# Kernel optimization log

Measured on AMD Instinct MI355X. Metric: run time of the kernel, lower is better.

The kernel has to match this reference:

```python
import jax, jax.numpy as jnp
import numpy as np
import math

T = 2048; HID = 2048; H = 16; KV = 8; G = H // KV; D = 128
GH = 128; BS = 64; NB = T // BS
EPS = 1e-6; RATIO = 0.2; SCALE = 1.0 / math.sqrt(D)


def _rope_tables(length, dim, theta=1000000.0):
    inv = 1.0 / (theta ** (np.arange(0, dim, 2, dtype=np.float32) / dim))
    f = np.outer(np.arange(length, dtype=np.float32), inv)
    emb = np.concatenate([f, f], axis=-1)
    return jnp.asarray(np.cos(emb)), jnp.asarray(np.sin(emb))


def _rot_half(x):
    d = x.shape[-1] // 2
    return jnp.concatenate([-x[..., d:], x[..., :d]], axis=-1)


def _apply_rope(x, cos, sin):
    # x: [T, nH, D], cos/sin: [T, D] broadcast over head dim
    return x * cos[:, None, :] + _rot_half(x) * sin[:, None, :]


def _rmsnorm(x, w, eps=EPS):
    xf = x.astype(jnp.float32)
    v = jnp.mean(xf * xf, axis=-1, keepdims=True)
    return (w * (xf * jax.lax.rsqrt(v + eps))).astype(x.dtype)


def setup_inputs() -> dict:
    key = jax.random.key(0)
    ks = jax.random.split(key, 8)
    s = 0.02
    hidden_states = jax.random.normal(ks[0], (T, HID), jnp.float32)
    Wq = jax.random.normal(ks[1], (HID, H * D), jnp.float32) * s
    Wk = jax.random.normal(ks[2], (HID, KV * D), jnp.float32) * s
    Wv = jax.random.normal(ks[3], (HID, KV * D), jnp.float32) * s
    Wo = jax.random.normal(ks[4], (H * D, HID), jnp.float32) * s
    q_norm_w = jnp.ones((D,), jnp.float32)
    k_norm_w = jnp.ones((D,), jnp.float32)
    gate_wq = jax.random.normal(ks[5], (D, GH), jnp.float32) * s
    gate_wk = jax.random.normal(ks[6], (D, GH), jnp.float32) * s
    cos, sin = _rope_tables(T, D)
    cos_gq, sin_gq = _rope_tables(T, GH)
    cos_blk, sin_blk = _rope_tables(NB, GH)
    # causal block mask: query t may attend to key block j iff j <= t // BS
    block_attention_mask = (jnp.arange(T)[:, None] // BS) >= jnp.arange(NB)[None, :]
    return dict(hidden_states=hidden_states, Wq=Wq, Wk=Wk, Wv=Wv, Wo=Wo,
                q_norm_w=q_norm_w, k_norm_w=k_norm_w, gate_wq=gate_wq, gate_wk=gate_wk,
                cos=cos, sin=sin, cos_gq=cos_gq, sin_gq=sin_gq,
                cos_blk=cos_blk, sin_blk=sin_blk,
                block_attention_mask=block_attention_mask)


def reference(hidden_states, Wq, Wk, Wv, Wo, q_norm_w, k_norm_w, gate_wq, gate_wk,
              cos, sin, cos_gq, sin_gq, cos_blk, sin_blk, block_attention_mask):
    q = (hidden_states @ Wq).reshape(T, H, D)
    k = (hidden_states @ Wk).reshape(T, KV, D)
    v = (hidden_states @ Wv).reshape(T, KV, D)
    q = _rmsnorm(q, q_norm_w)
    k = _rmsnorm(k, k_norm_w)

    # ---- gate network on un-roped q/k: q-head avg-pool to KV heads, k avg-pool per block ----
    q_pool = q.reshape(T, KV, G, D).mean(axis=2)            # [T, KV, D]
    gq = _apply_rope(q_pool @ gate_wq, cos_gq, sin_gq)      # [T, KV, GH]
    k_blk = k.reshape(NB, BS, KV, D).mean(axis=1)           # [NB, KV, D]
    gk = _apply_rope(k_blk @ gate_wk, cos_blk, sin_blk)     # [NB, KV, GH]
    gate_scores = jnp.einsum('tkg,nkg->ktn', gq, gk) / math.sqrt(GH)  # [KV, T, NB]
    predict_mask = jnp.where(block_attention_mask[None], gate_scores, -1e9)

    # ---- main attention (RoPE + GQA causal softmax attention) ----
    qr = _apply_rope(q, cos, sin)
    kr = _apply_rope(k, cos, sin)
    kr_rep = jnp.repeat(kr, G, axis=1)                      # [T, H, D]
    v_rep = jnp.repeat(v, G, axis=1)
    logits = jnp.einsum('thd,shd->hts', qr, kr_rep) * SCALE  # [H, T, T]
    causal = jnp.tril(jnp.ones((T, T), bool))
    logits = jnp.where(causal[None], logits, -jnp.inf)
    probs = jax.nn.softmax(logits, axis=-1)
    attn_output = jnp.einsum('hts,shd->thd', probs, v_rep).reshape(T, H * D) @ Wo

    # ---- pooled ground-truth block mask: attention mass per key block ----
    pooled = probs.reshape(H, T, NB, BS).sum(axis=-1)        # [H, T, NB]
    gt = pooled.reshape(KV, G, T, NB).max(axis=1)            # max_pool3d over head groups -> [KV,T,NB]
    gt = jnp.where(block_attention_mask[None], gt, 0.0)
    gt = gt / (gt.sum(axis=-1, keepdims=True) + 1e-9)

    # ---- KLDiv gate loss on the tail slice (bsz = 1) ----
    start = int(T * RATIO)
    tgt = gt[:, start:, :]                                   # [KV, L, NB]
    logp = jax.nn.log_softmax(predict_mask[:, start:, :], axis=-1)
    safe_t = jnp.where(tgt > 0, tgt, 1.0)
    kl = jnp.where(tgt > 0, tgt * (jnp.log(safe_t) - logp), 0.0)
    gate_loss = kl.reshape(KV, -1).mean(axis=-1).sum()       # KLDivLoss(reduction='mean') per kv head, summed, /bsz(=1)
    return attn_output, gate_loss
```

## Files before the change

### kernel.cpp

```cpp
#include <hip/hip_runtime.h>

#define T_ 2048
#define HID_ 2048
#define H_ 16
#define KV_ 8
#define G_ 2
#define D_ 128
#define GH_ 128
#define BS_ 64
#define NB_ 32
#define START_ 409
#define TG0_ 384
#define SCALE_ 0.08838834764831845f
#define MFIX_ 8.0f

typedef __attribute__((ext_vector_type(8))) short short8_t;
typedef __attribute__((ext_vector_type(4))) float float4_t;
typedef __attribute__((ext_vector_type(8))) unsigned short ushort8_t;
typedef __attribute__((ext_vector_type(4))) unsigned short ushort4_t;

__device__ __forceinline__ float wave_sum(float v) {
#pragma unroll
  for (int o = 32; o > 0; o >>= 1) v += __shfl_xor(v, o, 64);
  return v;
}
__device__ __forceinline__ unsigned short f2bf(float x) {
  unsigned int u = __float_as_uint(x);
  unsigned int r = (u + 0x7fffu + ((u >> 16) & 1u)) >> 16;
  return (unsigned short)r;
}

__device__ __forceinline__ void gload16(const void* g, void* l) {
  __builtin_amdgcn_global_load_lds((const __attribute__((address_space(1))) unsigned int*)g,
                                   (__attribute__((address_space(3))) unsigned int*)l, 16, 0, 0);
}

__device__ __forceinline__ void castT_dev(const float* __restrict__ in,
                                          unsigned short* __restrict__ out, int K, int N,
                                          int ldin, int bx, int by,
                                          unsigned short (*tile)[72], int tid) {
  int k0 = by * 64, n0 = bx * 64;
  int tx = tid & 63, ty4 = tid >> 6;
#pragma unroll
  for (int i = 0; i < 16; ++i) {
    int ky = ty4 * 16 + i;
    tile[tx][ky] = f2bf(in[(size_t)(k0 + ky) * ldin + n0 + tx]);
  }
  __syncthreads();
#pragma unroll
  for (int i = 0; i < 16; ++i) {
    int ny = ty4 * 16 + i;
    out[(size_t)(n0 + ny) * K + k0 + tx] = tile[ny][tx];
  }
}

__global__ __launch_bounds__(256) void castT(const float* __restrict__ in,
                                             unsigned short* __restrict__ out,
                                             int K, int N, int ldin) {
  __shared__ unsigned short tile[64][72];
  castT_dev(in, out, K, N, ldin, blockIdx.x, blockIdx.y, tile, threadIdx.x);
}

__global__ __launch_bounds__(256) void prep_cast(const float* __restrict__ hs,
                                                 const float* __restrict__ Wq,
                                                 const float* __restrict__ Wk,
                                                 const float* __restrict__ Wv,
                                                 const float* __restrict__ Wo,
                                                 const float* __restrict__ gwq,
                                                 const float* __restrict__ gwk,
                                                 unsigned short* __restrict__ hsb,
                                                 unsigned short* __restrict__ WqkvT,
                                                 unsigned short* __restrict__ WoT,
                                                 unsigned short* __restrict__ gwqT,
                                                 unsigned short* __restrict__ gwkT) {
  __shared__ unsigned short tile[64][72];
  int id = blockIdx.x, tid = threadIdx.x;
  if (id < 4096) {
    int i = id * 256 + tid;
    float4 v = ((const float4*)hs)[i];
    ushort4_t o = {f2bf(v.x), f2bf(v.y), f2bf(v.z), f2bf(v.w)};
    *(ushort4_t*)(hsb + (size_t)i * 4) = o;
  } else if (id < 5120) {
    int t = id - 4096;
    castT_dev(Wq, WqkvT, 2048, 2048, 2048, t & 31, t >> 5, tile, tid);
  } else if (id < 5632) {
    int t = id - 5120;
    castT_dev(Wk, WqkvT + (size_t)2048 * 2048, 2048, 1024, 1024, t & 15, t >> 4, tile, tid);
  } else if (id < 6144) {
    int t = id - 5632;
    castT_dev(Wv, WqkvT + (size_t)3072 * 2048, 2048, 1024, 1024, t & 15, t >> 4, tile, tid);
  } else if (id < 7168) {
    int t = id - 6144;
    castT_dev(Wo, WoT, 2048, 2048, 2048, t & 31, t >> 5, tile, tid);
  } else if (id < 7172) {
    int t = id - 7168;
    castT_dev(gwq, gwqT, 128, 128, 128, t & 1, t >> 1, tile, tid);
  } else {
    int t = id - 7172;
    castT_dev(gwk, gwkT, 128, 128, 128, t & 1, t >> 1, tile, tid);
  }
}

__global__ __launch_bounds__(256) void gemm_bf16_v3(const unsigned short* __restrict__ A,
                                                    const unsigned short* __restrict__ Bt,
                                                    float* __restrict__ C,
                                                    int M, int N, int K, int ldc) {
  __shared__ unsigned short As[128 * 64];
  __shared__ unsigned short Bs[128 * 64];
  int tid = threadIdx.x;
  int wid = tid >> 6, lane = tid & 63;
  int quad = lane >> 4, l16 = lane & 15;
  int wm = wid & 1, wn = wid >> 1;
  int m0 = blockIdx.y * 128, n0 = blockIdx.x * 128;
  const unsigned short* gA[4];
  const unsigned short* gB[4];
#pragma unroll
  for (int it = 0; it < 4; ++it) {
    int line = wid * 32 + it * 8 + (lane >> 3);
    int chunk = (lane & 7) ^ (line & 7);
    gA[it] = A + (size_t)(m0 + line) * K + chunk * 8;
    gB[it] = Bt + (size_t)(n0 + line) * K + chunk * 8;
  }
  float4_t acc[4][4];
#pragma unroll
  for (int i = 0; i < 4; ++i)
#pragma unroll
    for (int j = 0; j < 4; ++j) acc[i][j] = (float4_t){0.f, 0.f, 0.f, 0.f};
  for (int k0 = 0; k0 < K; k0 += 64) {
    __syncthreads();
#pragma unroll
    for (int it = 0; it < 4; ++it) {
      gload16(gA[it] + k0, As + (wid * 32 + it * 8) * 64);
      gload16(gB[it] + k0, Bs + (wid * 32 + it * 8) * 64);
    }
    __syncthreads();
    short8_t a[2][4], b[2][4];
#pragma unroll
    for (int ks = 0; ks < 2; ++ks) {
      int sw = ((ks * 4 + quad) ^ (l16 & 7)) * 8;
#pragma unroll
      for (int i = 0; i < 4; ++i) {
        a[ks][i] = *(const short8_t*)&As[(wm * 64 + i * 16 + l16) * 64 + sw];
        b[ks][i] = *(const short8_t*)&Bs[(wn * 64 + i * 16 + l16) * 64 + sw];
      }
    }
#pragma unroll
    for (int ks = 0; ks < 2; ++ks)
#pragma unroll
      for (int i = 0; i < 4; ++i)
#pragma unroll
        for (int j = 0; j < 4; ++j)
          acc[i][j] = __builtin_amdgcn_mfma_f32_16x16x32_bf16(a[ks][i], b[ks][j], acc[i][j], 0, 0, 0);
  }
#pragma unroll
  for (int i = 0; i < 4; ++i)
#pragma unroll
    for (int j = 0; j < 4; ++j)
#pragma unroll
      for (int reg = 0; reg < 4; ++reg)
        C[(size_t)(m0 + wm * 64 + i * 16 + quad * 4 + reg) * ldc + n0 + wn * 64 + j * 16 + l16] =
            acc[i][j][reg];
}

__global__ __launch_bounds__(128) void norm_rope_fused(const float* __restrict__ qkvf,
                                                       const float* __restrict__ qw,
                                                       const float* __restrict__ kw,
                                                       const float* __restrict__ cosT,
                                                       const float* __restrict__ sinT,
                                                       unsigned short* __restrict__ qbf,
                                                       unsigned short* __restrict__ qpool_bf,
                                                       unsigned short* __restrict__ kbf,
                                                       float* __restrict__ knorm) {
  int t = blockIdx.x, d = threadIdx.x;
  if (blockIdx.y < 8) {
    int kv = blockIdx.y;
    size_t i0 = (size_t)t * 4096 + (kv * G_) * D_ + d;
    float x0 = qkvf[i0], x1 = qkvf[i0 + D_];
    __shared__ float sred[2][2];
    float s0 = wave_sum(x0 * x0), s1 = wave_sum(x1 * x1);
    if ((d & 63) == 0) { sred[0][d >> 6] = s0; sred[1][d >> 6] = s1; }
    __syncthreads();
    float wv = qw[d];
    float n0 = x0 * rsqrtf((sred[0][0] + sred[0][1]) * (1.f / D_) + 1e-6f) * wv;
    float n1 = x1 * rsqrtf((sred[1][0] + sred[1][1]) * (1.f / D_) + 1e-6f) * wv;
    if (t >= TG0_) qpool_bf[((size_t)(t - TG0_) * KV_ + kv) * D_ + d] = f2bf(0.5f * (n0 + n1));
    __shared__ float sh[2][D_];
    sh[0][d] = n0; sh[1][d] = n1;
    __syncthreads();
    float c = cosT[t * D_ + d], s = sinT[t * D_ + d];
    float r0 = (d < 64) ? -sh[0][d + 64] : sh[0][d - 64];
    float r1 = (d < 64) ? -sh[1][d + 64] : sh[1][d - 64];
    qbf[((size_t)(t * H_) + kv * G_) * D_ + d] = f2bf(n0 * c + r0 * s);
    qbf[((size_t)(t * H_) + kv * G_ + 1) * D_ + d] = f2bf(n1 * c + r1 * s);
  } else {
    int kv = blockIdx.y - 8;
    float x = qkvf[(size_t)t * 4096 + 2048 + kv * D_ + d];
    __shared__ float sredk[2];
    float s0 = wave_sum(x * x);
    if ((d & 63) == 0) sredk[d >> 6] = s0;
    __syncthreads();
    float nk = x * rsqrtf((sredk[0] + sredk[1]) * (1.f / D_) + 1e-6f) * kw[d];
    knorm[(size_t)(t * KV_ + kv) * D_ + d] = nk;
    __shared__ float shk[D_];
    shk[d] = nk;
    __syncthreads();
    float rot = (d < 64) ? -shk[d + 64] : shk[d - 64];
    kbf[(size_t)(t * KV_ + kv) * D_ + d] = f2bf(nk * cosT[t * D_ + d] + rot * sinT[t * D_ + d]);
  }
}

__global__ __launch_bounds__(128) void kblk_kernel(const float* __restrict__ knorm,
                                                   unsigned short* __restrict__ kblk_bf) {
  int n = blockIdx.x, kv = blockIdx.y, d = threadIdx.x;
  float s = 0.f;
  for (int i = 0; i < BS_; ++i) s += knorm[((size_t)(n * BS_ + i) * KV_ + kv) * D_ + d];
  kblk_bf[(size_t)(n * KV_ + kv) * D_ + d] = f2bf(s * (1.f / BS_));
}

__global__ __launch_bounds__(128) void rope_g_fused(float* __restrict__ gq, float* __restrict__ gk,
                                                    const float* __restrict__ cosG,
                                                    const float* __restrict__ sinG,
                                                    const float* __restrict__ cosB,
                                                    const float* __restrict__ sinB) {
  int r = blockIdx.x, kvh = blockIdx.y, d = threadIdx.x;
  float* x;
  size_t base;
  float c_, s_;
  if (r < NB_) {
    x = gk;
    base = (size_t)(r * KV_ + kvh) * GH_;
    c_ = cosB[r * GH_ + d]; s_ = sinB[r * GH_ + d];
  } else {
    int rr = r - NB_;
    x = gq;
    base = (size_t)(rr * KV_ + kvh) * GH_;
    c_ = cosG[(size_t)(TG0_ + rr) * GH_ + d]; s_ = sinG[(size_t)(TG0_ + rr) * GH_ + d];
  }
  __shared__ float sh[GH_];
  sh[d] = x[base + d];
  __syncthreads();
  float rot = (d < 64) ? -sh[d + 64] : sh[d - 64];
  x[base + d] = sh[d] * c_ + rot * s_;
}

__global__ __launch_bounds__(256) void attn_mfma(const unsigned short* __restrict__ qbf,
                                                 const unsigned short* __restrict__ kbf,
                                                 const unsigned short* __restrict__ vt,
                                                 unsigned short* __restrict__ attnb,
                                                 float* __restrict__ pooled) {
  int h = blockIdx.x;
  int yy = blockIdx.y;
  int tile = (yy < 16) ? yy : 47 - yy;
  int t0 = tile * 64;
  int tid = threadIdx.x;
  int wid = tid >> 6, lane = tid & 63;
  int quad = lane >> 4, l16 = lane & 15;
  int kv = h >> 1;
  __shared__ unsigned short Ks[2][64 * 128];
  __shared__ unsigned short Vs[2][128 * 64];
  __shared__ unsigned short Ps[4][16 * 72];

  const unsigned short* kbase[4];
  const unsigned short* vbase[4];
#pragma unroll
  for (int it = 0; it < 4; ++it) {
    int seg = wid * 4 + it;
    int krow = seg * 4 + (lane >> 4);
    int kchk = lane & 15;
    kbase[it] = kbf + ((size_t)krow * KV_ + kv) * D_ + ((kchk ^ (krow & 7)) << 3);
    int vrow = seg * 8 + (lane >> 3);
    int vchk = lane & 7;
    vbase[it] = vt + (size_t)(kv * 128 + vrow) * T_ + ((vchk ^ (vrow & 7)) << 3);
  }

  int tq = t0 + wid * 16 + l16;
  short8_t qf[4];
#pragma unroll
  for (int kb = 0; kb < 4; ++kb)
    qf[kb] = *(const short8_t*)&qbf[((size_t)tq * H_ + h) * D_ + kb * 32 + quad * 8];

  const short one_bf = (short)0x3F80;
  short8_t ones = {one_bf, one_bf, one_bf, one_bf, one_bf, one_bf, one_bf, one_bf};

  int tbase = t0 + wid * 16 + quad * 4;
  float l_[4] = {0.f, 0.f, 0.f, 0.f};
  float pacc[2][4] = {};
  float4_t o[8];
#pragma unroll
  for (int j = 0; j < 8; ++j) o[j] = (float4_t){0.f, 0.f, 0.f, 0.f};

  int nchunks = tile + 1;
#pragma unroll
  for (int it = 0; it < 4; ++it) {
    gload16(kbase[it], &Ks[0][(wid * 4 + it) * 512]);
    gload16(vbase[it], &Vs[0][(wid * 4 + it) * 512]);
  }
  for (int c = 0; c < nchunks; ++c) {
    __syncthreads();
    if (c + 1 < nchunks) {
      int b = (c + 1) & 1;
#pragma unroll
      for (int it = 0; it < 4; ++it) {
        gload16(kbase[it] + (size_t)(c + 1) * 65536, &Ks[b][(wid * 4 + it) * 512]);
        gload16(vbase[it] + (c + 1) * 64, &Vs[b][(wid * 4 + it) * 512]);
      }
    }
    const unsigned short* Ksc = Ks[c & 1];
    const unsigned short* Vsc = Vs[c & 1];

    float4_t s[4];
#pragma unroll
    for (int j = 0; j < 4; ++j) {
      float4_t a = (float4_t){0.f, 0.f, 0.f, 0.f};
#pragma unroll
      for (int kb = 0; kb < 4; ++kb) {
        short8_t kf = *(const short8_t*)&Ksc[(j * 16 + l16) * 128 + (((kb * 4 + quad) ^ (l16 & 7)) << 3)];
        a = __builtin_amdgcn_mfma_f32_16x16x32_bf16(qf[kb], kf, a, 0, 0, 0);
      }
      s[j] = a;
    }
    if (c == tile) {
#pragma unroll
      for (int reg = 0; reg < 4; ++reg) {
        int trow = tbase + reg;
#pragma unroll
        for (int j = 0; j < 4; ++j) {
          float p = __expf(s[j][reg] * SCALE_ - MFIX_);
          s[j][reg] = (c * 64 + j * 16 + l16 <= trow) ? p : 0.f;
        }
      }
    } else {
#pragma unroll
      for (int j = 0; j < 4; ++j)
#pragma unroll
        for (int reg = 0; reg < 4; ++reg)
          s[j][reg] = __expf(s[j][reg] * SCALE_ - MFIX_);
    }
#pragma unroll
    for (int j = 0; j < 4; ++j)
#pragma unroll
      for (int reg = 0; reg < 4; ++reg)
        Ps[wid][(quad * 4 + reg) * 72 + j * 16 + l16] = f2bf(s[j][reg]);
    float4_t pool = (float4_t){0.f, 0.f, 0.f, 0.f};
#pragma unroll
    for (int ks = 0; ks < 2; ++ks) {
      short8_t pf = *(const short8_t*)&Ps[wid][l16 * 72 + ks * 32 + quad * 8];
      pool = __builtin_amdgcn_mfma_f32_16x16x32_bf16(pf, ones, pool, 0, 0, 0);
#pragma unroll
      for (int jt = 0; jt < 8; ++jt) {
        short8_t vf = *(const short8_t*)&Vsc[(jt * 16 + l16) * 64 + (((ks * 4 + quad) ^ (l16 & 7)) << 3)];
        o[jt] = __builtin_amdgcn_mfma_f32_16x16x32_bf16(pf, vf, o[jt], 0, 0, 0);
      }
    }
    int half = c >> 4, cl = c & 15;
#pragma unroll
    for (int reg = 0; reg < 4; ++reg) {
      l_[reg] += pool[reg];
      if (l16 == cl) pacc[half][reg] = pool[reg];
    }
  }
  float inv[4];
#pragma unroll
  for (int reg = 0; reg < 4; ++reg) inv[reg] = 1.f / l_[reg];
#pragma unroll
  for (int jt = 0; jt < 8; ++jt)
#pragma unroll
    for (int reg = 0; reg < 4; ++reg)
      attnb[(size_t)(tbase + reg) * (H_ * D_) + h * D_ + jt * 16 + l16] =
          f2bf(o[jt][reg] * inv[reg]);
#pragma unroll
  for (int reg = 0; reg < 4; ++reg) {
    int trow = tbase + reg;
    pooled[((size_t)h * T_ + trow) * NB_ + l16] = pacc[0][reg] * inv[reg];
    pooled[((size_t)h * T_ + trow) * NB_ + 16 + l16] = pacc[1][reg] * inv[reg];
  }
}

__global__ __launch_bounds__(256) void gate_loss2(const float* __restrict__ gq,
                                                  const float* __restrict__ gk,
                                                  const float* __restrict__ pooled,
                                                  float* __restrict__ klsum) {
  int kv = blockIdx.x;
  int sub = threadIdx.x >> 5;
  int n = threadIdx.x & 31;
  int tloc = blockIdx.y * 8 + sub;
  bool act = tloc < (T_ - START_);
  int t = START_ + (act ? tloc : 0);
  const float4* a = (const float4*)(gq + ((size_t)(t - TG0_) * KV_ + kv) * GH_);
  const float4* b = (const float4*)(gk + (size_t)(n * KV_ + kv) * GH_);
  float dot = 0.f;
#pragma unroll
  for (int d4 = 0; d4 < 32; ++d4) {
    float4 av = a[d4], bv = b[d4];
    dot += av.x * bv.x + av.y * bv.y + av.z * bv.z + av.w * bv.w;
  }
  bool valid = (t / BS_) >= n;
  float score = valid ? dot * SCALE_ : -1e9f;
  float M = score;
#pragma unroll
  for (int o = 16; o > 0; o >>= 1) M = fmaxf(M, __shfl_xor(M, o, 64));
  float e = __expf(score - M);
  float Z = e;
#pragma unroll
  for (int o = 16; o > 0; o >>= 1) Z += __shfl_xor(Z, o, 64);
  float logZ = M + logf(Z);
  float g = 0.f;
  if (valid) {
    float p0 = pooled[((size_t)(kv * G_) * T_ + t) * NB_ + n];
    float p1 = pooled[((size_t)(kv * G_ + 1) * T_ + t) * NB_ + n];
    g = fmaxf(p0, p1);
  }
  float gs = g;
#pragma unroll
  for (int o = 16; o > 0; o >>= 1) gs += __shfl_xor(gs, o, 64);
  float tgt = g / (gs + 1e-9f);
  float kl = (tgt > 0.f) ? tgt * (logf(tgt) - (score - logZ)) : 0.f;
  float ks = kl;
#pragma unroll
  for (int o = 16; o > 0; o >>= 1) ks += __shfl_xor(ks, o, 64);
  if (n == 0 && act) klsum[kv * (T_ - START_) + tloc] = ks;
}

__global__ __launch_bounds__(256) void finalize_loss(const float* __restrict__ klsum,
                                                     float* __restrict__ out) {
  const int n = KV_ * (T_ - START_);
  float s = 0.f;
  for (int i = threadIdx.x; i < n; i += 256) s += klsum[i];
  s = wave_sum(s);
  __shared__ float sh[4];
  if ((threadIdx.x & 63) == 0) sh[threadIdx.x >> 6] = s;
  __syncthreads();
  if (threadIdx.x == 0)
    out[0] = (sh[0] + sh[1] + sh[2] + sh[3]) * (1.f / ((float)(T_ - START_) * NB_));
}

extern "C" void kernel_launch(void* const* d_in, const int* in_sizes, int n_in,
                              void* d_out, int out_size, void* d_ws, size_t ws_size,
                              hipStream_t stream) {
  const float* hs   = (const float*)d_in[0];
  const float* Wq   = (const float*)d_in[1];
  const float* Wk   = (const float*)d_in[2];
  const float* Wv   = (const float*)d_in[3];
  const float* Wo   = (const float*)d_in[4];
  const float* qw   = (const float*)d_in[5];
  const float* kw   = (const float*)d_in[6];
  const float* gwq  = (const float*)d_in[7];
  const float* gwk  = (const float*)d_in[8];
  const float* cosT = (const float*)d_in[9];
  const float* sinT = (const float*)d_in[10];
  const float* cosG = (const float*)d_in[11];
  const float* sinG = (const float*)d_in[12];
  const float* cosB = (const float*)d_in[13];
  const float* sinB = (const float*)d_in[14];
  float* out = (float*)d_out;
  float* ws = (float*)d_ws;
  const size_t MEG = 1048576;

  float*          qkvf     = ws;
  unsigned short* attnb    = (unsigned short*)ws;
  float*          pooled   = ws + 2 * MEG;
  float*          klsum    = ws + 3 * MEG;
  unsigned short* WqkvT    = (unsigned short*)(ws + 8 * MEG);
  unsigned short* qbf      = WqkvT;
  unsigned short* kbf      = WqkvT + 4 * MEG;
  unsigned short* vt       = WqkvT + 6 * MEG;
  unsigned short* hsb      = (unsigned short*)(ws + 12 * MEG);
  float*          knorm    = ws + 12 * MEG;
  unsigned short* WoT      = (unsigned short*)(ws + 14 * MEG);
  unsigned short* qpool_bf = (unsigned short*)(ws + 16 * MEG);
  float*          gq       = ws + 17 * MEG;
  unsigned short* kblk_bf  = (unsigned short*)(ws + 18 * MEG + 786432);
  float*          gk       = ws + 18 * MEG + 819200;
  unsigned short* gwqT     = (unsigned short*)(ws + 18 * MEG + 851968);
  unsigned short* gwkT     = (unsigned short*)(ws + 18 * MEG + 860160);

  prep_cast<<<7176, 256, 0, stream>>>(hs, Wq, Wk, Wv, Wo, gwq, gwk, hsb, WqkvT, WoT, gwqT, gwkT);
  gemm_bf16_v3<<<dim3(32, 16), 256, 0, stream>>>(hsb, WqkvT, qkvf, 2048, 4096, 2048, 4096);
  norm_rope_fused<<<dim3(T_, 16), 128, 0, stream>>>(qkvf, qw, kw, cosT, sinT, qbf, qpool_bf,
                                                    kbf, knorm);
  castT<<<dim3(16, 32), 256, 0, stream>>>(qkvf + 3072, vt, T_, 1024, 4096);
  kblk_kernel<<<dim3(NB_, KV_), 128, 0, stream>>>(knorm, kblk_bf);
  gemm_bf16_v3<<<dim3(1, 104), 256, 0, stream>>>(qpool_bf, gwqT, gq, 13312, 128, 128, 128);
  gemm_bf16_v3<<<dim3(1, 2), 256, 0, stream>>>(kblk_bf, gwkT, gk, 256, 128, 128, 128);
  rope_g_fused<<<dim3(NB_ + (T_ - TG0_), KV_), 128, 0, stream>>>(gq, gk, cosG, sinG, cosB, sinB);
  attn_mfma<<<dim3(H_, 32), 256, 0, stream>>>(qbf, kbf, vt, attnb, pooled);
  gemm_bf16_v3<<<dim3(16, 16), 256, 0, stream>>>(attnb, WoT, out, 2048, 2048, 2048, 2048);
  gate_loss2<<<dim3(KV_, 205), 256, 0, stream>>>(gq, gk, pooled, klsum);
  finalize_loss<<<1, 256, 0, stream>>>(klsum, out + (size_t)T_ * HID_);
}
```

Before: 361.6 us.

## Split attention KV chunks across two blocks and merge partial outputs

Each query tile now runs as two blocks that take alternating key chunks (even and odd). Each block writes unnormalised bf16 partial outputs and row sums, and a new merge kernel adds the two halves and normalises. Blocks drop to 2 waves, each handling 32 query rows so that K/V fragments are reused across two row sets. Double-buffered async loads are replaced by a single buffer behind two barriers. The intent is more parallelism and better balance of the causal workload, at the cost of an extra kernel, extra partial-output memory traffic, bf16 rounding of the partials, and less load/compute overlap.

```diff
diff --git a/kernel.cpp b/kernel.cpp
--- a/kernel.cpp
+++ b/kernel.cpp
@@ -13,6 +13,7 @@
 #define TG0_ 384
 #define SCALE_ 0.08838834764831845f
 #define MFIX_ 8.0f
+#define HT_ 32768
 
 typedef __attribute__((ext_vector_type(8))) short short8_t;
 typedef __attribute__((ext_vector_type(4))) float float4_t;
@@ -28,6 +29,9 @@
   unsigned int u = __float_as_uint(x);
   unsigned int r = (u + 0x7fffu + ((u >> 16) & 1u)) >> 16;
   return (unsigned short)r;
+}
+__device__ __forceinline__ float bf2f(unsigned short h) {
+  return __uint_as_float(((unsigned int)h) << 16);
 }
 
 __device__ __forceinline__ void gload16(const void* g, void* l) {
@@ -243,28 +247,36 @@
   x[base + d] = sh[d] * c_ + rot * s_;
 }
 
-__global__ __launch_bounds__(256) void attn_mfma(const unsigned short* __restrict__ qbf,
-                                                 const unsigned short* __restrict__ kbf,
-                                                 const unsigned short* __restrict__ vt,
-                                                 unsigned short* __restrict__ attnb,
-                                                 float* __restrict__ pooled) {
+__global__ __launch_bounds__(128, 2) void attn_mfma(const unsigned short* __restrict__ qbf,
+                                                    const unsigned short* __restrict__ kbf,
+                                                    const unsigned short* __restrict__ vt,
+                                                    unsigned short* __restrict__ opart,
+                                                    float* __restrict__ lpart,
+                                                    float* __restrict__ pooledraw) {
   int h = blockIdx.x;
-  int yy = blockIdx.y;
-  int tile = (yy < 16) ? yy : 47 - yy;
+  int y = blockIdx.y;
+  int tile, p;
+  {
+    int qd = y >> 4, r = y & 15;
+    if (qd == 0)      { tile = r;       p = 0; }
+    else if (qd == 1) { tile = 16 + r;  p = 0; }
+    else if (qd == 2) { tile = 15 - r;  p = 1; }
+    else              { tile = 31 - r;  p = 1; }
+  }
   int t0 = tile * 64;
   int tid = threadIdx.x;
   int wid = tid >> 6, lane = tid & 63;
   int quad = lane >> 4, l16 = lane & 15;
   int kv = h >> 1;
-  __shared__ unsigned short Ks[2][64 * 128];
-  __shared__ unsigned short Vs[2][128 * 64];
-  __shared__ unsigned short Ps[4][16 * 72];
-
-  const unsigned short* kbase[4];
-  const unsigned short* vbase[4];
-#pragma unroll
-  for (int it = 0; it < 4; ++it) {
-    int seg = wid * 4 + it;
+  __shared__ unsigned short Ks[64 * 128];
+  __shared__ unsigned short Vs[128 * 64];
+  __shared__ unsigned short Ps[2][32 * 64];
+
+  const unsigned short* kbase[8];
+  const unsigned short* vbase[8];
+#pragma unroll
+  for (int it = 0; it < 8; ++it) {
+    int seg = wid * 8 + it;
     int krow = seg * 4 + (lane >> 4);
     int kchk = lane & 15;
     kbase[it] = kbf + ((size_t)krow * KV_ + kv) * D_ + ((kchk ^ (krow & 7)) << 3);
@@ -273,112 +285,160 @@
     vbase[it] = vt + (size_t)(kv * 128 + vrow) * T_ + ((vchk ^ (vrow & 7)) << 3);
   }
 
-  int tq = t0 + wid * 16 + l16;
-  short8_t qf[4];
-#pragma unroll
-  for (int kb = 0; kb < 4; ++kb)
-    qf[kb] = *(const short8_t*)&qbf[((size_t)tq * H_ + h) * D_ + kb * 32 + quad * 8];
+  short8_t qf[2][4];
+#pragma unroll
+  for (int rs = 0; rs < 2; ++rs) {
+    int tq = t0 + wid * 32 + rs * 16 + l16;
+#pragma unroll
+    for (int kb = 0; kb < 4; ++kb)
+      qf[rs][kb] = *(const short8_t*)&qbf[((size_t)tq * H_ + h) * D_ + kb * 32 + quad * 8];
+  }
 
   const short one_bf = (short)0x3F80;
   short8_t ones = {one_bf, one_bf, one_bf, one_bf, one_bf, one_bf, one_bf, one_bf};
 
-  int tbase = t0 + wid * 16 + quad * 4;
-  float l_[4] = {0.f, 0.f, 0.f, 0.f};
-  float pacc[2][4] = {};
-  float4_t o[8];
-#pragma unroll
-  for (int j = 0; j < 8; ++j) o[j] = (float4_t){0.f, 0.f, 0.f, 0.f};
-
-  int nchunks = tile + 1;
-#pragma unroll
-  for (int it = 0; it < 4; ++it) {
-    gload16(kbase[it], &Ks[0][(wid * 4 + it) * 512]);
-    gload16(vbase[it], &Vs[0][(wid * 4 + it) * 512]);
-  }
-  for (int c = 0; c < nchunks; ++c) {
-    __syncthreads();
-    if (c + 1 < nchunks) {
-      int b = (c + 1) & 1;
-#pragma unroll
-      for (int it = 0; it < 4; ++it) {
-        gload16(kbase[it] + (size_t)(c + 1) * 65536, &Ks[b][(wid * 4 + it) * 512]);
-        gload16(vbase[it] + (c + 1) * 64, &Vs[b][(wid * 4 + it) * 512]);
-      }
+  float l_[2][4] = {};
+  float pacc[2][2][4] = {};
+  float4_t o[2][8];
+#pragma unroll
+  for (int rs = 0; rs < 2; ++rs)
+#pragma unroll
+    for (int j = 0; j < 8; ++j) o[rs][j] = (float4_t){0.f, 0.f, 0.f, 0.f};
+
+  for (int c = p; c <= tile; c += 2) {
+    __syncthreads();
+#pragma unroll
+    for (int it = 0; it < 8; ++it) {
+      gload16(kbase[it] + (size_t)c * 65536, Ks + (wid * 8 + it) * 512);
+      gload16(vbase[it] + c * 64, Vs + (wid * 8 + it) * 512);
     }
-    const unsigned short* Ksc = Ks[c & 1];
-    const unsigned short* Vsc = Vs[c & 1];
-
-    float4_t s[4];
+    __syncthreads();
+
+    float4_t s[4][2];
 #pragma unroll
     for (int j = 0; j < 4; ++j) {
-      float4_t a = (float4_t){0.f, 0.f, 0.f, 0.f};
-#pragma unroll
-      for (int kb = 0; kb < 4; ++kb) {
-        short8_t kf = *(const short8_t*)&Ksc[(j * 16 + l16) * 128 + (((kb * 4 + quad) ^ (l16 & 7)) << 3)];
-        a = __builtin_amdgcn_mfma_f32_16x16x32_bf16(qf[kb], kf, a, 0, 0, 0);
-      }
-      s[j] = a;
+      short8_t kf[4];
+#pragma unroll
+      for (int kb = 0; kb < 4; ++kb)
+        kf[kb] = *(const short8_t*)&Ks[(j * 16 + l16) * 128 + (((kb * 4 + quad) ^ (l16 & 7)) << 3)];
+#pragma unroll
+      for (int rs = 0; rs < 2; ++rs) {
+        float4_t a = (float4_t){0.f, 0.f, 0.f, 0.f};
+#pragma unroll
+        for (int kb = 0; kb < 4; ++kb)
+          a = __builtin_amdgcn_mfma_f32_16x16x32_bf16(qf[rs][kb], kf[kb], a, 0, 0, 0);
+        s[j][rs] = a;
+      }
     }
     if (c == tile) {
 #pragma unroll
+      for (int rs = 0; rs < 2; ++rs)
+#pragma unroll
+        for (int reg = 0; reg < 4; ++reg) {
+          int trow = t0 + wid * 32 + rs * 16 + quad * 4 + reg;
+#pragma unroll
+          for (int j = 0; j < 4; ++j) {
+            float pv = __expf(s[j][rs][reg] * SCALE_ - MFIX_);
+            s[j][rs][reg] = (c * 64 + j * 16 + l16 <= trow) ? pv : 0.f;
+          }
+        }
+    } else {
+#pragma unroll
+      for (int j = 0; j < 4; ++j)
+#pragma unroll
+        for (int rs = 0; rs < 2; ++rs)
+#pragma unroll
+          for (int reg = 0; reg < 4; ++reg)
+            s[j][rs][reg] = __expf(s[j][rs][reg] * SCALE_ - MFIX_);
+    }
+#pragma unroll
+    for (int j = 0; j < 4; ++j)
+#pragma unroll
+      for (int rs = 0; rs < 2; ++rs)
+#pragma unroll
+        for (int reg = 0; reg < 4; ++reg) {
+          int rr = rs * 16 + quad * 4 + reg;
+          Ps[wid][rr * 64 + ((((j * 2) + (l16 >> 3)) ^ (rr & 7)) << 3) + (l16 & 7)] =
+              f2bf(s[j][rs][reg]);
+        }
+    float4_t pool[2];
+    pool[0] = (float4_t){0.f, 0.f, 0.f, 0.f};
+    pool[1] = (float4_t){0.f, 0.f, 0.f, 0.f};
+#pragma unroll
+    for (int ks = 0; ks < 2; ++ks) {
+      short8_t pf[2];
+#pragma unroll
+      for (int rs = 0; rs < 2; ++rs) {
+        int rr = rs * 16 + l16;
+        pf[rs] = *(const short8_t*)&Ps[wid][rr * 64 + (((ks * 4 + quad) ^ (rr & 7)) << 3)];
+        pool[rs] = __builtin_amdgcn_mfma_f32_16x16x32_bf16(pf[rs], ones, pool[rs], 0, 0, 0);
+      }
+#pragma unroll
+      for (int jt = 0; jt < 8; ++jt) {
+        short8_t vf = *(const short8_t*)&Vs[(jt * 16 + l16) * 64 + (((ks * 4 + quad) ^ (l16 & 7)) << 3)];
+#pragma unroll
+        for (int rs = 0; rs < 2; ++rs)
+          o[rs][jt] = __builtin_amdgcn_mfma_f32_16x16x32_bf16(pf[rs], vf, o[rs][jt], 0, 0, 0);
+      }
+    }
+    int half16 = (c >> 4) & 1, cl = c & 15;
+#pragma unroll
+    for (int rs = 0; rs < 2; ++rs)
+#pragma unroll
       for (int reg = 0; reg < 4; ++reg) {
-        int trow = tbase + reg;
-#pragma unroll
-        for (int j = 0; j < 4; ++j) {
-          float p = __expf(s[j][reg] * SCALE_ - MFIX_);
-          s[j][reg] = (c * 64 + j * 16 + l16 <= trow) ? p : 0.f;
-        }
-      }
-    } else {
-#pragma unroll
-      for (int j = 0; j < 4; ++j)
-#pragma unroll
-        for (int reg = 0; reg < 4; ++reg)
-          s[j][reg] = __expf(s[j][reg] * SCALE_ - MFIX_);
-    }
-#pragma unroll
-    for (int j = 0; j < 4; ++j)
-#pragma unroll
-      for (int reg = 0; reg < 4; ++reg)
-        Ps[wid][(quad * 4 + reg) * 72 + j * 16 + l16] = f2bf(s[j][reg]);
-    float4_t pool = (float4_t){0.f, 0.f, 0.f, 0.f};
-#pragma unroll
-    for (int ks = 0; ks < 2; ++ks) {
-      short8_t pf = *(const short8_t*)&Ps[wid][l16 * 72 + ks * 32 + quad * 8];
-      pool = __builtin_amdgcn_mfma_f32_16x16x32_bf16(pf, ones, pool, 0, 0, 0);
-#pragma unroll
-      for (int jt = 0; jt < 8; ++jt) {
-        short8_t vf = *(const short8_t*)&Vsc[(jt * 16 + l16) * 64 + (((ks * 4 + quad) ^ (l16 & 7)) << 3)];
-        o[jt] = __builtin_amdgcn_mfma_f32_16x16x32_bf16(pf, vf, o[jt], 0, 0, 0);
-      }
-    }
-    int half = c >> 4, cl = c & 15;
-#pragma unroll
-    for (int reg = 0; reg < 4; ++reg) {
-      l_[reg] += pool[reg];
-      if (l16 == cl) pacc[half][reg] = pool[reg];
-    }
-  }
-  float inv[4];
-#pragma unroll
-  for (int reg = 0; reg < 4; ++reg) inv[reg] = 1.f / l_[reg];
-#pragma unroll
-  for (int jt = 0; jt < 8; ++jt)
-#pragma unroll
-    for (int reg = 0; reg < 4; ++reg)
-      attnb[(size_t)(tbase + reg) * (H_ * D_) + h * D_ + jt * 16 + l16] =
-          f2bf(o[jt][reg] * inv[reg]);
-#pragma unroll
-  for (int reg = 0; reg < 4; ++reg) {
-    int trow = tbase + reg;
-    pooled[((size_t)h * T_ + trow) * NB_ + l16] = pacc[0][reg] * inv[reg];
-    pooled[((size_t)h * T_ + trow) * NB_ + 16 + l16] = pacc[1][reg] * inv[reg];
-  }
+        l_[rs][reg] += pool[rs][reg];
+        if (l16 == cl) pacc[half16][rs][reg] = pool[rs][reg];
+      }
+  }
+  unsigned short* op = opart + (size_t)p * (T_ * H_ * D_);
+#pragma unroll
+  for (int rs = 0; rs < 2; ++rs)
+#pragma unroll
+    for (int jt = 0; jt < 8; ++jt)
+#pragma unroll
+      for (int reg = 0; reg < 4; ++reg) {
+        int trow = t0 + wid * 32 + rs * 16 + quad * 4 + reg;
+        op[(size_t)trow * (H_ * D_) + h * D_ + jt * 16 + l16] = f2bf(o[rs][jt][reg]);
+      }
+  if (l16 == 0) {
+#pragma unroll
+    for (int rs = 0; rs < 2; ++rs)
+#pragma unroll
+      for (int reg = 0; reg < 4; ++reg) {
+        int trow = t0 + wid * 32 + rs * 16 + quad * 4 + reg;
+        lpart[p * HT_ + h * T_ + trow] = l_[rs][reg];
+      }
+  }
+  if ((l16 & 1) == p) {
+#pragma unroll
+    for (int rs = 0; rs < 2; ++rs)
+#pragma unroll
+      for (int reg = 0; reg < 4; ++reg) {
+        int trow = t0 + wid * 32 + rs * 16 + quad * 4 + reg;
+        pooledraw[((size_t)h * T_ + trow) * NB_ + l16] = pacc[0][rs][reg];
+        pooledraw[((size_t)h * T_ + trow) * NB_ + 16 + l16] = pacc[1][rs][reg];
+      }
+  }
+}
+
+__global__ __launch_bounds__(256) void merge_o(const unsigned short* __restrict__ opart,
+                                               const float* __restrict__ lpart,
+                                               unsigned short* __restrict__ attnb) {
+  int i = (blockIdx.x * 256 + threadIdx.x) * 4;
+  int t = i >> 11, h = (i & 2047) >> 7;
+  float inv = 1.f / (lpart[h * T_ + t] + lpart[HT_ + h * T_ + t]);
+  ushort4_t a = *(const ushort4_t*)(opart + i);
+  ushort4_t b = *(const ushort4_t*)(opart + (size_t)(T_ * H_ * D_) + i);
+  ushort4_t r;
+#pragma unroll
+  for (int k = 0; k < 4; ++k) r[k] = f2bf((bf2f(a[k]) + bf2f(b[k])) * inv);
+  *(ushort4_t*)(attnb + i) = r;
 }
 
 __global__ __launch_bounds__(256) void gate_loss2(const float* __restrict__ gq,
                                                   const float* __restrict__ gk,
-                                                  const float* __restrict__ pooled,
+                                                  const float* __restrict__ pooledraw,
+                                                  const float* __restrict__ lpart,
                                                   float* __restrict__ klsum) {
   int kv = blockIdx.x;
   int sub = threadIdx.x >> 5;
@@ -406,8 +466,11 @@
   float logZ = M + logf(Z);
   float g = 0.f;
   if (valid) {
-    float p0 = pooled[((size_t)(kv * G_) * T_ + t) * NB_ + n];
-    float p1 = pooled[((size_t)(kv * G_ + 1) * T_ + t) * NB_ + n];
+    int h0 = kv * G_, h1 = h0 + 1;
+    float inv0 = 1.f / (lpart[h0 * T_ + t] + lpart[HT_ + h0 * T_ + t]);
+    float inv1 = 1.f / (lpart[h1 * T_ + t] + lpart[HT_ + h1 * T_ + t]);
+    float p0 = pooledraw[((size_t)h0 * T_ + t) * NB_ + n] * inv0;
+    float p1 = pooledraw[((size_t)h1 * T_ + t) * NB_ + n] * inv1;
     g = fmaxf(p0, p1);
   }
   float gs = g;
@@ -456,23 +519,25 @@
   float* ws = (float*)d_ws;
   const size_t MEG = 1048576;
 
-  float*          qkvf     = ws;
-  unsigned short* attnb    = (unsigned short*)ws;
-  float*          pooled   = ws + 2 * MEG;
-  float*          klsum    = ws + 3 * MEG;
-  unsigned short* WqkvT    = (unsigned short*)(ws + 8 * MEG);
-  unsigned short* qbf      = WqkvT;
-  unsigned short* kbf      = WqkvT + 4 * MEG;
-  unsigned short* vt       = WqkvT + 6 * MEG;
-  unsigned short* hsb      = (unsigned short*)(ws + 12 * MEG);
-  float*          knorm    = ws + 12 * MEG;
-  unsigned short* WoT      = (unsigned short*)(ws + 14 * MEG);
-  unsigned short* qpool_bf = (unsigned short*)(ws + 16 * MEG);
-  float*          gq       = ws + 17 * MEG;
-  unsigned short* kblk_bf  = (unsigned short*)(ws + 18 * MEG + 786432);
-  float*          gk       = ws + 18 * MEG + 819200;
-  unsigned short* gwqT     = (unsigned short*)(ws + 18 * MEG + 851968);
-  unsigned short* gwkT     = (unsigned short*)(ws + 18 * MEG + 860160);
+  float*          qkvf      = ws;
+  unsigned short* opart     = (unsigned short*)ws;
+  unsigned short* attnb     = (unsigned short*)(ws + 4 * MEG);
+  float*          pooledraw = ws + 6 * MEG;
+  float*          lpart     = ws + 7 * MEG;
+  float*          klsum     = ws + 7 * MEG + 65536;
+  unsigned short* WqkvT     = (unsigned short*)(ws + 8 * MEG);
+  unsigned short* qbf       = WqkvT;
+  unsigned short* kbf       = WqkvT + 4 * MEG;
+  unsigned short* vt        = WqkvT + 6 * MEG;
+  unsigned short* hsb       = (unsigned short*)(ws + 12 * MEG);
+  float*          knorm     = ws + 12 * MEG;
+  unsigned short* WoT       = (unsigned short*)(ws + 14 * MEG);
+  unsigned short* qpool_bf  = (unsigned short*)(ws + 16 * MEG);
+  float*          gq        = ws + 17 * MEG;
+  unsigned short* kblk_bf   = (unsigned short*)(ws + 18 * MEG + 786432);
+  float*          gk        = ws + 18 * MEG + 819200;
+  unsigned short* gwqT      = (unsigned short*)(ws + 18 * MEG + 851968);
+  unsigned short* gwkT      = (unsigned short*)(ws + 18 * MEG + 860160);
 
   prep_cast<<<7176, 256, 0, stream>>>(hs, Wq, Wk, Wv, Wo, gwq, gwk, hsb, WqkvT, WoT, gwqT, gwkT);
   gemm_bf16_v3<<<dim3(32, 16), 256, 0, stream>>>(hsb, WqkvT, qkvf, 2048, 4096, 2048, 4096);
@@ -483,8 +548,9 @@
   gemm_bf16_v3<<<dim3(1, 104), 256, 0, stream>>>(qpool_bf, gwqT, gq, 13312, 128, 128, 128);
   gemm_bf16_v3<<<dim3(1, 2), 256, 0, stream>>>(kblk_bf, gwkT, gk, 256, 128, 128, 128);
   rope_g_fused<<<dim3(NB_ + (T_ - TG0_), KV_), 128, 0, stream>>>(gq, gk, cosG, sinG, cosB, sinB);
-  attn_mfma<<<dim3(H_, 32), 256, 0, stream>>>(qbf, kbf, vt, attnb, pooled);
+  attn_mfma<<<dim3(H_, 64), 128, 0, stream>>>(qbf, kbf, vt, opart, lpart, pooledraw);
+  merge_o<<<4096, 256, 0, stream>>>(opart, lpart, attnb);
   gemm_bf16_v3<<<dim3(16, 16), 256, 0, stream>>>(attnb, WoT, out, 2048, 2048, 2048, 2048);
-  gate_loss2<<<dim3(KV_, 205), 256, 0, stream>>>(gq, gk, pooled, klsum);
+  gate_loss2<<<dim3(KV_, 205), 256, 0, stream>>>(gq, gk, pooledraw, lpart, klsum);
   finalize_loss<<<1, 256, 0, stream>>>(klsum, out + (size_t)T_ * HID_);
 }
```

New measurement: 367.4 us. No clear change (+1.6%).
